# Performance work log

Measured on AMD Instinct MI355X. Metric: run time of the kernel, lower is better.

The kernel has to match this reference:

```python
import jax, jax.numpy as jnp
import numpy as np

EPS = 1e-10
B = 524288
NSTATE = 68

PARAM_NAMES = [
    'ka1','kr1','kc1','kpCraf','kpMek','kpErk','kDegradEgfr','kErkInbEgfr','kShcDephos','kptpDeg',
    'kGrb2CombShc','kSprtyInbGrb2','kSosCombGrb2','kErkPhosSos','kErkPhosPcraf','kPcrafDegrad',
    'kErkPhosMek','kMekDegrad','kDuspInbErk','kErkDeg','kinbBraf','kDuspStop','kDusps','kSproutyForm',
    'kSprtyComeDown','kdegrad','km_Sprty_decay','km_Dusp','km_Sprty','kErkDephos','kDuspDeg',
    'kHer2_act','kHer3_act','k_p85_bind_EGFR','k_p85_bind_Her2','k_p85_bind_Her3','k_p85_bind_IGFR',
    'k_p85_unbind','k_PI3K_recruit','kMTOR_Feedback','k_PIP2_to_PIP3','k_PTEN','kAkt','kdegradAKT',
    'kb1','k43b1','k4ebp1','k_4EBP1_dephos','kKSRphos','kKSRdephos','kMekByBraf','kMekByCraf',
    'kMekByKSR','Tram','K_tram_RAF','K_tram_KSR','n_tram','Vemurafenib','kDimerForm','kDimerDissoc',
    'kParadoxCRAF','IC50_vem','Hill_n_vem','kPDGFR_act','k_p85_bind_PDGFR','kS6K_phos','kS6K_dephos',
    'kRAS_PI3K','kERK_IRS_inhibit','kERK_PTEN_activate','kAKT_CRAF_inhibit','kS6K_IRS_inhibit',
    'kERK_GAB1_inhibit','kAKT_TSC2_phos','kERK_RSK_activate']

PARAM_DEFAULTS = [
    0.1,0.05,0.2,0.1,0.1,0.1,0.01,0.01,0.05,0.01,
    0.1,0.01,0.1,0.01,0.01,0.01,
    0.01,0.01,0.05,0.01,0.01,0.01,0.1,0.1,
    0.01,0.01,0.01,0.1,0.1,0.05,0.01,
    0.05,0.05,0.1,0.1,0.1,0.1,
    0.05,0.1,0.01,0.1,0.05,0.1,0.01,
    0.05,0.05,0.1,0.05,0.1,0.05,0.1,0.1,
    0.05,0.1,1.0,1.0,1.0,1.0,0.1,0.05,
    0.1,1.0,1.0,0.05,0.1,0.1,0.05,
    0.05,0.02,0.01,0.02,0.02,
    0.01,0.05,0.03]

assert len(PARAM_NAMES) == len(PARAM_DEFAULTS) == 75


def _rhs(t, y, params):
    p = {n: params[i] for i, n in enumerate(PARAM_NAMES)}
    Y = jnp.clip(y, 0.0)
    ys = [Y[..., i] for i in range(NSTATE)]
    d = [None] * NSTATE
    # --- EGFR / Her2 / Her3 receptor modules ---
    d[0] = -p['ka1']*ys[0] + p['kr1']*ys[1]
    d[1] = p['ka1']*ys[0] - p['kr1']*ys[1] - p['kc1']*ys[1]
    d[2] = p['kc1']*ys[1] - p['kDegradEgfr']*ys[2] - p['kErkInbEgfr']*ys[28]*ys[2]
    d[3] = -p['kHer2_act']*ys[3] + p['kr1']*ys[4]
    d[4] = p['kHer2_act']*ys[3] - p['kr1']*ys[4] - p['kc1']*ys[4]
    d[5] = p['kc1']*ys[4] - p['kDegradEgfr']*ys[5] - p['kErkInbEgfr']*ys[28]*ys[5]
    d[6] = -p['kHer3_act']*ys[6] + p['kr1']*ys[7]
    d[7] = p['kHer3_act']*ys[6] - p['kr1']*ys[7] - p['kc1']*ys[7]
    d[8] = p['kc1']*ys[7] - p['kDegradEgfr']*ys[8] - p['kErkInbEgfr']*ys[28]*ys[8]
    # --- Shc / Grb2 / Sos / Ras ---
    d[9] = -p['ka1']*ys[2]*ys[9]
    d[10] = p['ka1']*ys[2]*ys[9] - p['kShcDephos']*ys[11]*ys[10]
    d[11] = -p['kptpDeg']*ys[10]*ys[11]
    d[12] = p['kGrb2CombShc']*ys[10]*ys[2] - p['kSprtyInbGrb2']*ys[26]*ys[12]
    d[13] = p['kSosCombGrb2']*ys[12]*ys[10] - p['kErkPhosSos']*ys[24]*ys[13]
    d[14] = -p['ka1']*ys[13]*ys[14]
    d[15] = p['ka1']*ys[13]*ys[14]
    d[16] = -p['ka1']*ys[13]*ys[16]
    d[17] = p['ka1']*ys[13]*ys[16]
    d[18] = -p['ka1']*ys[13]*ys[18]
    d[19] = p['ka1']*ys[13]*ys[18] - p['ka1']*ys[19]*ys[20]
    d[20] = -p['ka1']*ys[19]*ys[20]
    # --- RAF with vemurafenib paradox ---
    IC50_n = p['IC50_vem'] ** p['Hill_n_vem']
    Vem_n = p['Vemurafenib'] ** p['Hill_n_vem']
    kBRAF_eff = p['ka1'] * IC50_n / (IC50_n + Vem_n + EPS)
    paradox = p['kParadoxCRAF'] * p['Vemurafenib'] * ys[61]
    akt_inh_craf = p['kAKT_CRAF_inhibit']*ys[52]*ys[21]
    d[21] = (-p['kpCraf']*ys[19]*ys[21] + p['kErkPhosPcraf']*ys[28]*ys[22]
             + p['kPcrafDegrad']*ys[22]*ys[35]
             - p['kDimerForm']*ys[24]*ys[21]*p['Vemurafenib'] + p['kDimerDissoc']*ys[61]
             - akt_inh_craf)
    d[22] = (p['kpCraf']*ys[19]*ys[21] - p['kErkPhosPcraf']*ys[28]*ys[22]
             - p['kPcrafDegrad']*ys[22]*ys[35] + paradox)
    d[23] = (-kBRAF_eff*ys[23]*ys[19] - p['kDimerForm']*ys[24]*ys[21]*p['Vemurafenib']
             + p['kDimerDissoc']*ys[61])
    d[24] = (kBRAF_eff*ys[23]*ys[19] - p['kinbBraf']*ys[24]
             - p['kDimerForm']*ys[24]*ys[21]*p['Vemurafenib'] + p['kDimerDissoc']*ys[61])
    d[61] = (p['kDimerForm']*ys[24]*ys[21]*p['Vemurafenib'] - p['kDimerDissoc']*ys[61]
             - p['kPcrafDegrad']*ys[61]*ys[35])
    # --- MEK / ERK ---
    raf_to_mek = p['kpMek']*ys[22] + p['kMekByBraf']*ys[24] + p['kMekByCraf']*ys[22]
    ksr_to_mek = p['kMekByKSR']*ys[60]
    d[25] = -(raf_to_mek + ksr_to_mek)*ys[25] + p['kErkPhosMek']*ys[28]*ys[26] + p['kMekDegrad']*ys[26]*ys[34]
    d[26] = (raf_to_mek + ksr_to_mek)*ys[25] - p['kErkPhosMek']*ys[28]*ys[26] - p['kMekDegrad']*ys[26]*ys[34]
    d[27] = (-p['kpErk']*ys[26]*ys[27] + p['kDuspInbErk']*ys[30]*ys[28]
             + p['kErkDeg']*ys[28]*ys[33] + p['kErkDephos']*ys[30]*ys[28])
    d[28] = (p['kpErk']*ys[26]*ys[27] - p['kDuspInbErk']*ys[30]*ys[28]
             - p['kErkDeg']*ys[28]*ys[33] - p['kErkDephos']*ys[30]*ys[28])
    # --- DUSP / Sprouty feedback ---
    denom_dusp = 1 + p['km_Dusp'] / (p['kDusps'] + EPS) * ys[28]
    d[29] = p['km_Dusp']*ys[28]/(denom_dusp + EPS) - p['kDuspStop']*ys[29]*ys[36] - p['kDuspDeg']*ys[29]*ys[28]
    d[30] = -p['kDuspStop']*ys[29]*ys[30]
    denom_spry = 1 + p['km_Sprty'] / (p['kSproutyForm'] + EPS) * ys[28]
    d[31] = p['km_Sprty']*ys[28]/(denom_spry + EPS) - p['kSprtyComeDown']*ys[31]*ys[32]
    d[32] = -p['kSprtyComeDown']*ys[31]*ys[32]
    d[33] = -p['kErkDeg']*ys[28]*ys[33]
    d[34] = -p['kMekDegrad']*ys[26]*ys[34]
    d[35] = -p['kPcrafDegrad']*ys[22]*ys[35]
    d[36] = -p['kDuspStop']*ys[29]*ys[36]
    # --- IGFR / IRS ---
    d[37] = -p['ka1']*ys[37] + p['kr1']*ys[38]
    d[38] = p['ka1']*ys[37] - p['kr1']*ys[38] - p['kc1']*ys[38]
    d[39] = p['kc1']*ys[38] - p['kErkInbEgfr']*ys[28]*ys[39]
    erk_irs = p['kERK_IRS_inhibit']*ys[28]*ys[41]
    s6k_irs = p['kS6K_IRS_inhibit']*ys[66]*ys[41]
    d[40] = -p['ka1']*ys[2]*ys[40] + erk_irs + s6k_irs
    d[41] = p['ka1']*ys[2]*ys[40] - erk_irs - s6k_irs
    # --- p85 binding ---
    gab1 = 1.0 / (1.0 + p['kERK_GAB1_inhibit']*ys[28])
    d[42] = (-p['k_p85_bind_EGFR']*ys[2]*ys[42]*gab1
             - p['k_p85_bind_Her2']*ys[5]*ys[42]*gab1
             - p['k_p85_bind_Her3']*ys[8]*ys[42]*gab1
             - p['k_p85_bind_IGFR']*ys[39]*ys[42]
             - p['k_p85_bind_PDGFR']*ys[64]*ys[42]
             + p['k_p85_unbind']*(ys[43] + ys[44] + ys[45] + ys[46] + ys[67]))
    d[43] = p['k_p85_bind_EGFR']*ys[2]*ys[42]*gab1 - p['k_p85_unbind']*ys[43]
    d[44] = p['k_p85_bind_Her2']*ys[5]*ys[42]*gab1 - p['k_p85_unbind']*ys[44]
    d[45] = p['k_p85_bind_Her3']*ys[8]*ys[42]*gab1 - p['k_p85_unbind']*ys[45]
    d[46] = p['k_p85_bind_IGFR']*ys[39]*ys[42] - p['k_p85_unbind']*ys[46]
    d[67] = p['k_p85_bind_PDGFR']*ys[64]*ys[42] - p['k_p85_unbind']*ys[67]
    # --- PI3K/AKT/mTOR axis (reconstructed; source truncated) ---
    total_p85c = ys[43] + ys[44] + ys[45] + ys[46] + ys[67]
    pi3k_act = p['k_PI3K_recruit']*total_p85c*ys[47] + p['kRAS_PI3K']*ys[15]*ys[47]
    mtor_fb = p['kMTOR_Feedback']*ys[56]*ys[48]
    d[47] = -pi3k_act + mtor_fb
    d[48] = pi3k_act - mtor_fb
    d[49] = -p['k_PIP2_to_PIP3']*ys[48]*ys[49] + p['k_PTEN']*ys[51]*ys[50]
    d[50] = p['k_PIP2_to_PIP3']*ys[48]*ys[49] - p['k_PTEN']*ys[51]*ys[50]
    d[51] = p['kERK_PTEN_activate']*ys[28] - p['kdegrad']*ys[51]
    d[52] = p['kAkt']*ys[50]*ys[53] - p['kdegradAKT']*ys[52]
    d[53] = -p['kAkt']*ys[50]*ys[53] + p['kdegradAKT']*ys[52]
    d[54] = -p['kAKT_TSC2_phos']*ys[52]*ys[54]
    d[55] = p['kAKT_TSC2_phos']*ys[52]*ys[54] - p['kdegrad']*ys[55]
    d[56] = p['kb1']*ys[52]*ys[57] - p['k43b1']*ys[56]
    d[57] = -p['kb1']*ys[52]*ys[57] + p['k43b1']*ys[56]
    d[58] = -p['k4ebp1']*ys[56]*ys[58] + p['k_4EBP1_dephos']*ys[59]
    d[59] = p['k4ebp1']*ys[56]*ys[58] - p['k_4EBP1_dephos']*ys[59]
    # --- KSR with trametinib hill factor (reconstructed) ---
    Ktram_n = p['K_tram_KSR'] ** p['n_tram']
    tram_n = p['Tram'] ** p['n_tram']
    tram_ksr = Ktram_n / (Ktram_n + tram_n + EPS)
    d[60] = p['kKSRphos']*ys[19]*ys[62]*tram_ksr - p['kKSRdephos']*ys[60]
    d[62] = -p['kKSRphos']*ys[19]*ys[62]*tram_ksr + p['kKSRdephos']*ys[60]
    # --- PDGFR (reconstructed) ---
    d[63] = -p['kPDGFR_act']*ys[63]
    d[64] = p['kPDGFR_act']*ys[63] - p['kDegradEgfr']*ys[64]
    # --- S6K (reconstructed) ---
    d[65] = -p['kS6K_phos']*ys[56]*ys[65] + p['kS6K_dephos']*ys[66] - p['kERK_RSK_activate']*ys[28]*ys[65]
    d[66] = p['kS6K_phos']*ys[56]*ys[65] - p['kS6K_dephos']*ys[66] + p['kERK_RSK_activate']*ys[28]*ys[65]
    return jnp.stack(d, axis=-1)


def setup_inputs() -> dict:
    key = jax.random.key(0)
    k1, _ = jax.random.split(key)
    y = jax.random.uniform(k1, (B, NSTATE), dtype=jnp.float32)  # nonnegative concentrations
    t = jnp.zeros((1,), dtype=jnp.float32)
    params = jnp.asarray(PARAM_DEFAULTS, dtype=jnp.float32)
    return {'t': t, 'y': y, 'params': params}


def reference(t, y, params):
    return _rhs(t, y, params)
```

## Files before the change

### kernel.cpp

```cpp
#include <hip/hip_runtime.h>
#include <math.h>

#define NS 68
#define NSP 69
#define BLOCK 128
#define WAVE 64
#define F4_PER_ROW 17
#define F4_PER_WAVE (WAVE * F4_PER_ROW)
#define EPSC 1e-10f

__global__ __launch_bounds__(BLOCK) void MAPKPI3KODE_rhs_kernel(
    const float* __restrict__ y,
    const float* __restrict__ params,
    float* __restrict__ out)
{
    __shared__ float sm[(BLOCK / WAVE) * WAVE * NSP];
    const int t    = threadIdx.x;
    const int wid  = t >> 6;
    const int lane = t & 63;
    float* wsm = &sm[wid * WAVE * NSP];

    const int wave_base4 = (blockIdx.x * (BLOCK / WAVE) + wid) * F4_PER_WAVE;

    const float4* __restrict__ y4 = (const float4*)y;
    #pragma unroll
    for (int k = 0; k < F4_PER_ROW; ++k) {
        int g = k * WAVE + lane;
        float4 v = y4[wave_base4 + g];
        int row = g / F4_PER_ROW;
        int c4  = g - row * F4_PER_ROW;
        float* dst = &wsm[row * NSP + 4 * c4];
        dst[0] = v.x; dst[1] = v.y; dst[2] = v.z; dst[3] = v.w;
    }

    float Y[NS];
    {
        const float* my = &wsm[lane * NSP];
        #pragma unroll
        for (int i = 0; i < NS; ++i) Y[i] = fmaxf(my[i], 0.0f);
    }

    const float ka1             = params[0];
    const float kr1             = params[1];
    const float kc1             = params[2];
    const float kpCraf          = params[3];
    const float kpMek           = params[4];
    const float kpErk           = params[5];
    const float kDegradEgfr     = params[6];
    const float kErkInbEgfr     = params[7];
    const float kShcDephos      = params[8];
    const float kptpDeg         = params[9];
    const float kGrb2CombShc    = params[10];
    const float kSprtyInbGrb2   = params[11];
    const float kSosCombGrb2    = params[12];
    const float kErkPhosSos     = params[13];
    const float kErkPhosPcraf   = params[14];
    const float kPcrafDegrad    = params[15];
    const float kErkPhosMek     = params[16];
    const float kMekDegrad      = params[17];
    const float kDuspInbErk     = params[18];
    const float kErkDeg         = params[19];
    const float kinbBraf        = params[20];
    const float kDuspStop       = params[21];
    const float kDusps          = params[22];
    const float kSproutyForm    = params[23];
    const float kSprtyComeDown  = params[24];
    const float kdegrad         = params[25];
    const float km_Dusp         = params[27];
    const float km_Sprty        = params[28];
    const float kErkDephos      = params[29];
    const float kDuspDeg        = params[30];
    const float kHer2_act       = params[31];
    const float kHer3_act       = params[32];
    const float k_p85_bind_EGFR = params[33];
    const float k_p85_bind_Her2 = params[34];
    const float k_p85_bind_Her3 = params[35];
    const float k_p85_bind_IGFR = params[36];
    const float k_p85_unbind    = params[37];
    const float k_PI3K_recruit  = params[38];
    const float kMTOR_Feedback  = params[39];
    const float k_PIP2_to_PIP3  = params[40];
    const float k_PTEN          = params[41];
    const float kAkt            = params[42];
    const float kdegradAKT      = params[43];
    const float kb1             = params[44];
    const float k43b1           = params[45];
    const float k4ebp1          = params[46];
    const float k_4EBP1_dephos  = params[47];
    const float kKSRphos        = params[48];
    const float kKSRdephos      = params[49];
    const float kMekByBraf      = params[50];
    const float kMekByCraf      = params[51];
    const float kMekByKSR       = params[52];
    const float Tram            = params[53];
    const float K_tram_KSR      = params[55];
    const float n_tram          = params[56];
    const float Vemurafenib     = params[57];
    const float kDimerForm      = params[58];
    const float kDimerDissoc    = params[59];
    const float kParadoxCRAF    = params[60];
    const float IC50_vem        = params[61];
    const float Hill_n_vem      = params[62];
    const float kPDGFR_act      = params[63];
    const float k_p85_bind_PDGFR= params[64];
    const float kS6K_phos       = params[65];
    const float kS6K_dephos     = params[66];
    const float kRAS_PI3K       = params[67];
    const float kERK_IRS_inhibit   = params[68];
    const float kERK_PTEN_activate = params[69];
    const float kAKT_CRAF_inhibit  = params[70];
    const float kS6K_IRS_inhibit   = params[71];
    const float kERK_GAB1_inhibit  = params[72];
    const float kAKT_TSC2_phos     = params[73];
    const float kERK_RSK_activate  = params[74];

    const float IC50_n   = powf(IC50_vem, Hill_n_vem);
    const float Vem_n    = powf(Vemurafenib, Hill_n_vem);
    const float kBRAF_eff = ka1 * IC50_n / (IC50_n + Vem_n + EPSC);
    const float Ktram_n  = powf(K_tram_KSR, n_tram);
    const float tram_n   = powf(Tram, n_tram);
    const float tram_ksr = Ktram_n / (Ktram_n + tram_n + EPSC);

    float d[NS];

    d[0] = -ka1*Y[0] + kr1*Y[1];
    d[1] =  ka1*Y[0] - kr1*Y[1] - kc1*Y[1];
    d[2] =  kc1*Y[1] - kDegradEgfr*Y[2] - kErkInbEgfr*Y[28]*Y[2];
    d[3] = -kHer2_act*Y[3] + kr1*Y[4];
    d[4] =  kHer2_act*Y[3] - kr1*Y[4] - kc1*Y[4];
    d[5] =  kc1*Y[4] - kDegradEgfr*Y[5] - kErkInbEgfr*Y[28]*Y[5];
    d[6] = -kHer3_act*Y[6] + kr1*Y[7];
    d[7] =  kHer3_act*Y[6] - kr1*Y[7] - kc1*Y[7];
    d[8] =  kc1*Y[7] - kDegradEgfr*Y[8] - kErkInbEgfr*Y[28]*Y[8];
    d[9]  = -ka1*Y[2]*Y[9];
    d[10] =  ka1*Y[2]*Y[9] - kShcDephos*Y[11]*Y[10];
    d[11] = -kptpDeg*Y[10]*Y[11];
    d[12] =  kGrb2CombShc*Y[10]*Y[2] - kSprtyInbGrb2*Y[26]*Y[12];
    d[13] =  kSosCombGrb2*Y[12]*Y[10] - kErkPhosSos*Y[24]*Y[13];
    d[14] = -ka1*Y[13]*Y[14];
    d[15] =  ka1*Y[13]*Y[14];
    d[16] = -ka1*Y[13]*Y[16];
    d[17] =  ka1*Y[13]*Y[16];
    d[18] = -ka1*Y[13]*Y[18];
    d[19] =  ka1*Y[13]*Y[18] - ka1*Y[19]*Y[20];
    d[20] = -ka1*Y[19]*Y[20];
    {
        const float paradox = kParadoxCRAF * Vemurafenib * Y[61];
        const float akt_inh_craf = kAKT_CRAF_inhibit * Y[52] * Y[21];
        const float dimf = kDimerForm * Y[24] * Y[21] * Vemurafenib;
        const float dimd = kDimerDissoc * Y[61];
        d[21] = -kpCraf*Y[19]*Y[21] + kErkPhosPcraf*Y[28]*Y[22]
                + kPcrafDegrad*Y[22]*Y[35]
                - dimf + dimd - akt_inh_craf;
        d[22] =  kpCraf*Y[19]*Y[21] - kErkPhosPcraf*Y[28]*Y[22]
                - kPcrafDegrad*Y[22]*Y[35] + paradox;
        d[23] = -kBRAF_eff*Y[23]*Y[19] - dimf + dimd;
        d[24] =  kBRAF_eff*Y[23]*Y[19] - kinbBraf*Y[24] - dimf + dimd;
        d[61] =  dimf - dimd - kPcrafDegrad*Y[61]*Y[35];
    }
    {
        const float raf_to_mek = kpMek*Y[22] + kMekByBraf*Y[24] + kMekByCraf*Y[22];
        const float ksr_to_mek = kMekByKSR*Y[60];
        const float to_mek = (raf_to_mek + ksr_to_mek) * Y[25];
        d[25] = -to_mek + kErkPhosMek*Y[28]*Y[26] + kMekDegrad*Y[26]*Y[34];
        d[26] =  to_mek - kErkPhosMek*Y[28]*Y[26] - kMekDegrad*Y[26]*Y[34];
        d[27] = -kpErk*Y[26]*Y[27] + kDuspInbErk*Y[30]*Y[28]
                + kErkDeg*Y[28]*Y[33] + kErkDephos*Y[30]*Y[28];
        d[28] =  kpErk*Y[26]*Y[27] - kDuspInbErk*Y[30]*Y[28]
                - kErkDeg*Y[28]*Y[33] - kErkDephos*Y[30]*Y[28];
    }
    {
        const float denom_dusp = 1.0f + km_Dusp / (kDusps + EPSC) * Y[28];
        d[29] = km_Dusp*Y[28]/(denom_dusp + EPSC) - kDuspStop*Y[29]*Y[36] - kDuspDeg*Y[29]*Y[28];
        d[30] = -kDuspStop*Y[29]*Y[30];
        const float denom_spry = 1.0f + km_Sprty / (kSproutyForm + EPSC) * Y[28];
        d[31] = km_Sprty*Y[28]/(denom_spry + EPSC) - kSprtyComeDown*Y[31]*Y[32];
        d[32] = -kSprtyComeDown*Y[31]*Y[32];
        d[33] = -kErkDeg*Y[28]*Y[33];
        d[34] = -kMekDegrad*Y[26]*Y[34];
        d[35] = -kPcrafDegrad*Y[22]*Y[35];
        d[36] = -kDuspStop*Y[29]*Y[36];
    }
    d[37] = -ka1*Y[37] + kr1*Y[38];
    d[38] =  ka1*Y[37] - kr1*Y[38] - kc1*Y[38];
    d[39] =  kc1*Y[38] - kErkInbEgfr*Y[28]*Y[39];
    {
        const float erk_irs = kERK_IRS_inhibit*Y[28]*Y[41];
        const float s6k_irs = kS6K_IRS_inhibit*Y[66]*Y[41];
        d[40] = -ka1*Y[2]*Y[40] + erk_irs + s6k_irs;
        d[41] =  ka1*Y[2]*Y[40] - erk_irs - s6k_irs;
    }
    {
        const float gab1 = 1.0f / (1.0f + kERK_GAB1_inhibit*Y[28]);
        const float bE = k_p85_bind_EGFR*Y[2]*Y[42]*gab1;
        const float b2 = k_p85_bind_Her2*Y[5]*Y[42]*gab1;
        const float b3 = k_p85_bind_Her3*Y[8]*Y[42]*gab1;
        const float bI = k_p85_bind_IGFR*Y[39]*Y[42];
        const float bP = k_p85_bind_PDGFR*Y[64]*Y[42];
        const float total_p85c = Y[43] + Y[44] + Y[45] + Y[46] + Y[67];
        d[42] = -bE - b2 - b3 - bI - bP + k_p85_unbind*total_p85c;
        d[43] = bE - k_p85_unbind*Y[43];
        d[44] = b2 - k_p85_unbind*Y[44];
        d[45] = b3 - k_p85_unbind*Y[45];
        d[46] = bI - k_p85_unbind*Y[46];
        d[67] = bP - k_p85_unbind*Y[67];
        const float pi3k_act = k_PI3K_recruit*total_p85c*Y[47] + kRAS_PI3K*Y[15]*Y[47];
        const float mtor_fb  = kMTOR_Feedback*Y[56]*Y[48];
        d[47] = -pi3k_act + mtor_fb;
        d[48] =  pi3k_act - mtor_fb;
    }
    d[49] = -k_PIP2_to_PIP3*Y[48]*Y[49] + k_PTEN*Y[51]*Y[50];
    d[50] =  k_PIP2_to_PIP3*Y[48]*Y[49] - k_PTEN*Y[51]*Y[50];
    d[51] =  kERK_PTEN_activate*Y[28] - kdegrad*Y[51];
    d[52] =  kAkt*Y[50]*Y[53] - kdegradAKT*Y[52];
    d[53] = -kAkt*Y[50]*Y[53] + kdegradAKT*Y[52];
    d[54] = -kAKT_TSC2_phos*Y[52]*Y[54];
    d[55] =  kAKT_TSC2_phos*Y[52]*Y[54] - kdegrad*Y[55];
    d[56] =  kb1*Y[52]*Y[57] - k43b1*Y[56];
    d[57] = -kb1*Y[52]*Y[57] + k43b1*Y[56];
    d[58] = -k4ebp1*Y[56]*Y[58] + k_4EBP1_dephos*Y[59];
    d[59] =  k4ebp1*Y[56]*Y[58] - k_4EBP1_dephos*Y[59];
    d[60] =  kKSRphos*Y[19]*Y[62]*tram_ksr - kKSRdephos*Y[60];
    d[62] = -kKSRphos*Y[19]*Y[62]*tram_ksr + kKSRdephos*Y[60];
    d[63] = -kPDGFR_act*Y[63];
    d[64] =  kPDGFR_act*Y[63] - kDegradEgfr*Y[64];
    d[65] = -kS6K_phos*Y[56]*Y[65] + kS6K_dephos*Y[66] - kERK_RSK_activate*Y[28]*Y[65];
    d[66] =  kS6K_phos*Y[56]*Y[65] - kS6K_dephos*Y[66] + kERK_RSK_activate*Y[28]*Y[65];

    {
        float* my = &wsm[lane * NSP];
        #pragma unroll
        for (int i = 0; i < NS; ++i) my[i] = d[i];
    }

    float4* __restrict__ out4 = (float4*)out;
    #pragma unroll
    for (int k = 0; k < F4_PER_ROW; ++k) {
        int g = k * WAVE + lane;
        int row = g / F4_PER_ROW;
        int c4  = g - row * F4_PER_ROW;
        const float* src = &wsm[row * NSP + 4 * c4];
        float4 v;
        v.x = src[0]; v.y = src[1]; v.z = src[2]; v.w = src[3];
        out4[wave_base4 + g] = v;
    }
}

extern "C" void kernel_launch(void* const* d_in, const int* in_sizes, int n_in,
                              void* d_out, int out_size, void* d_ws, size_t ws_size,
                              hipStream_t stream) {
    const float* y      = (const float*)d_in[1];
    const float* params = (const float*)d_in[2];
    float* out          = (float*)d_out;

    const int rows   = in_sizes[1] / NS;
    const int blocks = rows / BLOCK;

    MAPKPI3KODE_rhs_kernel<<<blocks, BLOCK, 0, stream>>>(y, params, out);
}
```

Baseline: 254.7 us.

## Load rows directly into registers and stage output through half-size LDS buffer

Measured after the change: 290.2 us. 1.14x slower.

```diff
diff --git a/kernel.cpp b/kernel.cpp
--- a/kernel.cpp
+++ b/kernel.cpp
@@ -2,42 +2,39 @@
 #include <math.h>
 
 #define NS 68
-#define NSP 69
-#define BLOCK 128
+#define BLOCK 256
+#define WPB 4
 #define WAVE 64
 #define F4_PER_ROW 17
-#define F4_PER_WAVE (WAVE * F4_PER_ROW)
+#define HALFW 37
 #define EPSC 1e-10f
 
-__global__ __launch_bounds__(BLOCK) void MAPKPI3KODE_rhs_kernel(
+__global__ __launch_bounds__(BLOCK, 3) void MAPKPI3KODE_rhs_kernel(
     const float* __restrict__ y,
     const float* __restrict__ params,
     float* __restrict__ out)
 {
-    __shared__ float sm[(BLOCK / WAVE) * WAVE * NSP];
+    __shared__ float sm[WPB * WAVE * HALFW];
     const int t    = threadIdx.x;
     const int wid  = t >> 6;
     const int lane = t & 63;
-    float* wsm = &sm[wid * WAVE * NSP];
-
-    const int wave_base4 = (blockIdx.x * (BLOCK / WAVE) + wid) * F4_PER_WAVE;
+    float* wsm = &sm[wid * WAVE * HALFW];
+
+    const int wave_row0 = (blockIdx.x * WPB + wid) * WAVE;
+    const int row = wave_row0 + lane;
 
     const float4* __restrict__ y4 = (const float4*)y;
+    float4 v[F4_PER_ROW];
+    #pragma unroll
+    for (int k = 0; k < F4_PER_ROW; ++k) v[k] = y4[row * F4_PER_ROW + k];
+
+    float Y[NS];
     #pragma unroll
     for (int k = 0; k < F4_PER_ROW; ++k) {
-        int g = k * WAVE + lane;
-        float4 v = y4[wave_base4 + g];
-        int row = g / F4_PER_ROW;
-        int c4  = g - row * F4_PER_ROW;
-        float* dst = &wsm[row * NSP + 4 * c4];
-        dst[0] = v.x; dst[1] = v.y; dst[2] = v.z; dst[3] = v.w;
-    }
-
-    float Y[NS];
-    {
-        const float* my = &wsm[lane * NSP];
-        #pragma unroll
-        for (int i = 0; i < NS; ++i) Y[i] = fmaxf(my[i], 0.0f);
+        Y[4*k+0] = fmaxf(v[k].x, 0.0f);
+        Y[4*k+1] = fmaxf(v[k].y, 0.0f);
+        Y[4*k+2] = fmaxf(v[k].z, 0.0f);
+        Y[4*k+3] = fmaxf(v[k].w, 0.0f);
     }
 
     const float ka1             = params[0];
@@ -227,22 +224,31 @@
     d[65] = -kS6K_phos*Y[56]*Y[65] + kS6K_dephos*Y[66] - kERK_RSK_activate*Y[28]*Y[65];
     d[66] =  kS6K_phos*Y[56]*Y[65] - kS6K_dephos*Y[66] + kERK_RSK_activate*Y[28]*Y[65];
 
-    {
-        float* my = &wsm[lane * NSP];
-        #pragma unroll
-        for (int i = 0; i < NS; ++i) my[i] = d[i];
-    }
-
     float4* __restrict__ out4 = (float4*)out;
-    #pragma unroll
-    for (int k = 0; k < F4_PER_ROW; ++k) {
+    float* my = &wsm[lane * HALFW];
+
+    #pragma unroll
+    for (int i = 0; i < 32; ++i) my[i] = d[i];
+    #pragma unroll
+    for (int k = 0; k < 8; ++k) {
         int g = k * WAVE + lane;
-        int row = g / F4_PER_ROW;
-        int c4  = g - row * F4_PER_ROW;
-        const float* src = &wsm[row * NSP + 4 * c4];
-        float4 v;
-        v.x = src[0]; v.y = src[1]; v.z = src[2]; v.w = src[3];
-        out4[wave_base4 + g] = v;
+        int r = g >> 3;
+        int c = g & 7;
+        const float* src = &wsm[r * HALFW + 4 * c];
+        float4 o; o.x = src[0]; o.y = src[1]; o.z = src[2]; o.w = src[3];
+        out4[(wave_row0 + r) * F4_PER_ROW + c] = o;
+    }
+
+    #pragma unroll
+    for (int j = 0; j < 36; ++j) my[j] = d[32 + j];
+    #pragma unroll
+    for (int k = 0; k < 9; ++k) {
+        int g = k * WAVE + lane;
+        int r = g / 9;
+        int c = g - 9 * r;
+        const float* src = &wsm[r * HALFW + 4 * c];
+        float4 o; o.x = src[0]; o.y = src[1]; o.z = src[2]; o.w = src[3];
+        out4[(wave_row0 + r) * F4_PER_ROW + 8 + c] = o;
     }
 }
 
```
